# Kernel tuning notes

Measured on AMD Instinct MI355X. Metric: run time of the kernel, lower is better.

## Reference

```python
import jax, jax.numpy as jnp
import numpy as np

THETA = 10000.0


def apply_rope(x, theta):
    # x: [batch, heads, seq, head_dim], head_dim even
    d = x.shape[-1]
    s = x.shape[-2]
    freqs = 1.0 / (theta ** (jnp.arange(0, d, 2, dtype=jnp.float32) / d))  # [d/2]
    pos = jnp.arange(s, dtype=jnp.float32)
    ang = pos[:, None] * freqs[None, :]          # [seq, d/2]
    cos, sin = jnp.cos(ang), jnp.sin(ang)
    x_even = x[..., 0::2]
    x_odd = x[..., 1::2]
    r_even = x_even * cos - x_odd * sin
    r_odd = x_even * sin + x_odd * cos
    # interleave back: [..., seq, d/2, 2] -> [..., seq, d]
    out = jnp.stack([r_even, r_odd], axis=-1).reshape(x.shape)
    return out


def setup_inputs() -> dict:
    key = jax.random.key(0)
    ks = jax.random.split(key, 5)
    B, S, D = 2, 2048, 1024
    scale = 1.0 / np.sqrt(D)
    return {
        "x": jax.random.normal(ks[0], (B, S, D), dtype=jnp.float32),
        "q_proj_weight": jax.random.normal(ks[1], (D, D), dtype=jnp.float32) * scale,
        "k_proj_weight": jax.random.normal(ks[2], (D, D), dtype=jnp.float32) * scale,
        "v_proj_weight": jax.random.normal(ks[3], (D, D), dtype=jnp.float32) * scale,
        "o_proj_weight": jax.random.normal(ks[4], (D, D), dtype=jnp.float32) * scale,
    }


def reference(x, q_proj_weight, k_proj_weight, v_proj_weight, o_proj_weight):
    B, S, D = x.shape
    H = 16
    hd = D // H
    # projections: weight is (d_out, d_in)
    q = jnp.einsum('bsd,ed->bse', x, q_proj_weight)
    k = jnp.einsum('bsd,ed->bse', x, k_proj_weight)
    v = jnp.einsum('bsd,ed->bse', x, v_proj_weight)
    # split heads -> [B, H, S, hd]
    q = q.reshape(B, S, H, hd).transpose(0, 2, 1, 3)
    k = k.reshape(B, S, H, hd).transpose(0, 2, 1, 3)
    v = v.reshape(B, S, H, hd).transpose(0, 2, 1, 3)
    q = apply_rope(q, THETA)
    k = apply_rope(k, THETA)
    scores = jnp.einsum('bhqd,bhkd->bhqk', q, k) / jnp.sqrt(jnp.float32(hd))
    causal = jnp.tril(jnp.ones((S, S), dtype=bool))
    scores = jnp.where(causal, scores, -jnp.inf)
    attn = jax.nn.softmax(scores, axis=-1)
    out = jnp.einsum('bhqk,bhkd->bhqd', attn, v)
    out = out.transpose(0, 2, 1, 3).reshape(B, S, D)
    return jnp.einsum('bsv,dv->bsd', out, o_proj_weight)
```

## Files before the change

### kernel.cpp

```cpp
#include <hip/hip_runtime.h>
#include <hip/hip_bf16.h>
#include <stdint.h>

typedef __attribute__((ext_vector_type(4))) float f32x4;
typedef __attribute__((ext_vector_type(8))) __bf16 bf16x8;
typedef __attribute__((ext_vector_type(4))) __bf16 bf16x4;

#define DEVI __device__ __forceinline__

static constexpr int S_  = 2048;
static constexpr int D_  = 1024;
static constexpr int H_  = 16;
static constexpr int HD_ = 64;
static constexpr int M_  = 2 * S_;
static constexpr float SCL2 = 0.18033688f;

DEVI void gload_lds16(const void* gsrc, void* ldst) {
  __builtin_amdgcn_global_load_lds(
      (__attribute__((address_space(1))) void*)(void*)gsrc,
      (__attribute__((address_space(3))) void*)ldst, 16, 0, 0);
}

DEVI float fexp2(float x) {
  float r;
  asm("v_exp_f32 %0, %1" : "=v"(r) : "v"(x));
  return r;
}

__global__ __launch_bounds__(256) void cvt_all_kernel(
    const float* __restrict__ x, const float* __restrict__ wq,
    const float* __restrict__ wk, const float* __restrict__ wv,
    const float* __restrict__ wo,
    __bf16* __restrict__ xb, __bf16* __restrict__ wqb,
    __bf16* __restrict__ wkb, __bf16* __restrict__ wvb,
    __bf16* __restrict__ wob, float* __restrict__ tab) {
  int blk = blockIdx.x;
  if (blk < 8192) {
    int i = blk * 256 + threadIdx.x;
    const float* src; __bf16* dst; int off;
    if (i < (1 << 20))                      { src = x;  dst = xb;  off = 0; }
    else if (i < (1 << 20) + (1 << 18))     { src = wq; dst = wqb; off = (1 << 20); }
    else if (i < (1 << 20) + 2 * (1 << 18)) { src = wk; dst = wkb; off = (1 << 20) + (1 << 18); }
    else if (i < (1 << 20) + 3 * (1 << 18)) { src = wv; dst = wvb; off = (1 << 20) + 2 * (1 << 18); }
    else                                    { src = wo; dst = wob; off = (1 << 20) + 3 * (1 << 18); }
    int j = i - off;
    float4 v = reinterpret_cast<const float4*>(src)[j];
    bf16x4 o;
    o[0] = (__bf16)v.x; o[1] = (__bf16)v.y; o[2] = (__bf16)v.z; o[3] = (__bf16)v.w;
    reinterpret_cast<bf16x4*>(dst)[j] = o;
  } else {
    int i = (blk - 8192) * 256 + threadIdx.x;
    int s = i >> 5, f = i & 31;
    float freq = powf(10000.0f, -(float)(2 * f) / (float)HD_);
    float ang = (float)s * freq;
    tab[2 * i]     = cosf(ang);
    tab[2 * i + 1] = sinf(ang);
  }
}

__global__ __launch_bounds__(256) void gemm_qkv(
    const __bf16* __restrict__ A, const __bf16* __restrict__ W0,
    const __bf16* __restrict__ W1, const __bf16* __restrict__ W2,
    __bf16* __restrict__ Cq, __bf16* __restrict__ Ck, __bf16* __restrict__ Cvt,
    const float* __restrict__ tab) {
  __shared__ __attribute__((aligned(16))) __bf16 As[128 * 32];
  __shared__ __attribute__((aligned(16))) __bf16 Bs[128 * 32];
  const int tid  = threadIdx.x;
  const int lane = tid & 63;
  const int wv   = tid >> 6;
  const int m0 = blockIdx.x * 128;
  const int n0 = blockIdx.y * 128;
  const int z  = blockIdx.z;
  const __bf16* W = (z == 0) ? W0 : (z == 1 ? W1 : W2);
  const int wm = (wv >> 1) * 64, wn = (wv & 1) * 64;
  const int arow = lane & 15;
  const int kgrp = (lane >> 4) * 8;

  f32x4 acc[4][4];
#pragma unroll
  for (int i = 0; i < 4; i++)
#pragma unroll
    for (int j = 0; j < 4; j++) acc[i][j] = f32x4{0.f, 0.f, 0.f, 0.f};

  for (int k0 = 0; k0 < 1024; k0 += 32) {
    __syncthreads();
#pragma unroll
    for (int j = 0; j < 2; ++j) {
      int c   = (wv * 2 + j) * 64 + lane;
      int row = c >> 2;
      int kc  = (c & 3) * 8;
      gload_lds16(A + (size_t)(m0 + row) * 1024 + k0 + kc,
                  As + (size_t)(wv * 2 + j) * 512);
      gload_lds16(W + (size_t)(n0 + row) * 1024 + k0 + kc,
                  Bs + (size_t)(wv * 2 + j) * 512);
    }
    asm volatile("s_waitcnt vmcnt(0)" ::: "memory");
    __syncthreads();
    bf16x8 af[4], bw[4];
#pragma unroll
    for (int i = 0; i < 4; i++)
      af[i] = *reinterpret_cast<const bf16x8*>(As + (wm + i * 16 + arow) * 32 + kgrp);
#pragma unroll
    for (int i = 0; i < 4; i++)
      bw[i] = *reinterpret_cast<const bf16x8*>(Bs + (wn + i * 16 + arow) * 32 + kgrp);
#pragma unroll
    for (int i = 0; i < 4; i++)
#pragma unroll
      for (int j = 0; j < 4; j++)
        acc[i][j] = __builtin_amdgcn_mfma_f32_16x16x32_bf16(af[i], bw[j], acc[i][j], 0, 0, 0);
  }

  if (z == 2) {
#pragma unroll
    for (int i = 0; i < 4; i++) {
      int m = m0 + wm + i * 16 + (lane >> 4) * 4;
      int bb = m >> 11, srow = m & (S_ - 1);
#pragma unroll
      for (int j = 0; j < 4; j++) {
        int n = n0 + wn + j * 16 + arow;
        int h = n >> 6, d = n & 63;
        bf16x4 o4;
#pragma unroll
        for (int r = 0; r < 4; r++) o4[r] = (__bf16)acc[i][j][r];
        *reinterpret_cast<bf16x4*>(
            Cvt + ((size_t)(bb * H_ + h) * HD_ + d) * S_ + srow) = o4;
      }
    }
  } else {
#pragma unroll
    for (int i = 0; i < 4; i++) {
#pragma unroll
      for (int j = 0; j < 4; j++) {
#pragma unroll
        for (int r = 0; r < 4; r++) {
          int m = m0 + wm + i * 16 + (lane >> 4) * 4 + r;
          int n = n0 + wn + j * 16 + arow;
          float v = acc[i][j][r];
          int bb = m >> 11, srow = m & (S_ - 1);
          int h = n >> 6, d = n & 63;
          size_t oidx = ((size_t)(bb * H_ + h) * S_ + srow) * HD_ + d;
          float other = __shfl_xor(v, 1, 64);
          int fq = d >> 1;
          float2 cssn = *reinterpret_cast<const float2*>(tab + (srow * 32 + fq) * 2);
          float rv = (d & 1) ? (other * cssn.y + v * cssn.x)
                             : (v * cssn.x - other * cssn.y);
          if (z == 0) rv *= SCL2;
          ((z == 0) ? Cq : Ck)[oidx] = (__bf16)rv;
        }
      }
    }
  }
}

__global__ __launch_bounds__(256) void gemm_bt0(
    const __bf16* __restrict__ A, const __bf16* __restrict__ W0,
    float* __restrict__ Cf) {
  constexpr int BK = 32;
  __shared__ __attribute__((aligned(16))) __bf16 As[128 * BK];
  __shared__ __attribute__((aligned(16))) __bf16 Bs[128 * BK];
  const int tid  = threadIdx.x;
  const int lane = tid & 63;
  const int wv   = tid >> 6;
  const int m0 = blockIdx.x * 128;
  const int n0 = blockIdx.y * 128;
  const int wm = (wv >> 1) * 64, wn = (wv & 1) * 64;
  const int arow = lane & 15;
  const int kgrp = (lane >> 4) * 8;

  f32x4 acc[4][4];
#pragma unroll
  for (int i = 0; i < 4; i++)
#pragma unroll
    for (int j = 0; j < 4; j++) acc[i][j] = f32x4{0.f, 0.f, 0.f, 0.f};

  for (int k0 = 0; k0 < 1024; k0 += BK) {
    __syncthreads();
#pragma unroll
    for (int j = 0; j < 2; ++j) {
      int c   = (wv * 2 + j) * 64 + lane;
      int row = c >> 2;
      int kc  = (c & 3) * 8;
      gload_lds16(A + (size_t)(m0 + row) * 1024 + k0 + kc,
                  As + (size_t)(wv * 2 + j) * 512);
      gload_lds16(W0 + (size_t)(n0 + row) * 1024 + k0 + kc,
                  Bs + (size_t)(wv * 2 + j) * 512);
    }
    asm volatile("s_waitcnt vmcnt(0)" ::: "memory");
    __syncthreads();
    bf16x8 af[4], bw[4];
#pragma unroll
    for (int i = 0; i < 4; i++)
      af[i] = *reinterpret_cast<const bf16x8*>(As + (wm + i * 16 + arow) * BK + kgrp);
#pragma unroll
    for (int i = 0; i < 4; i++)
      bw[i] = *reinterpret_cast<const bf16x8*>(Bs + (wn + i * 16 + arow) * BK + kgrp);
#pragma unroll
    for (int i = 0; i < 4; i++)
#pragma unroll
      for (int j = 0; j < 4; j++)
        acc[i][j] = __builtin_amdgcn_mfma_f32_16x16x32_bf16(af[i], bw[j], acc[i][j], 0, 0, 0);
  }

#pragma unroll
  for (int i = 0; i < 4; i++)
#pragma unroll
    for (int j = 0; j < 4; j++)
#pragma unroll
      for (int r = 0; r < 4; r++) {
        int m = m0 + wm + i * 16 + (lane >> 4) * 4 + r;
        int n = n0 + wn + j * 16 + arow;
        Cf[(size_t)m * D_ + n] = acc[i][j][r];
      }
}

__global__ __launch_bounds__(256, 2) void attn_kernel(
    const __bf16* __restrict__ Q, const __bf16* __restrict__ K,
    const __bf16* __restrict__ Vt, __bf16* __restrict__ O) {
  __shared__ __attribute__((aligned(16))) __bf16 Ks[2][128 * 64];
  __shared__ __attribute__((aligned(16))) __bf16 Vs[2][64 * 128];
  const int tid = threadIdx.x, lane = tid & 63, wv = tid >> 6;
  const int bh = blockIdx.x;
  const int pr = blockIdx.y;
  const int b = bh >> 4, h = bh & 15;
  const __bf16* Qb  = Q  + (size_t)bh * S_ * HD_;
  const __bf16* Kb  = K  + (size_t)bh * S_ * HD_;
  const __bf16* Vtb = Vt + (size_t)bh * HD_ * S_;
  const int arow = lane & 15, g = lane >> 4;

#define STAGE(K0, BK_, BV_)                                                   \
  do {                                                                        \
    _Pragma("unroll") for (int j = 0; j < 4; ++j) {                           \
      int c = (wv * 4 + j) * 64 + lane;                    \
      int rowk = c >> 3, qqk = c & 7;                                         \
      int qsk = qqk ^ (rowk & 7);                                             \
      int ctp = rowk >> 4, rw = rowk & 15;                                    \
      int kph = ((ctp & 4) << 4) + ((ctp & 2) << 4) + ((ctp & 1) << 2)        \
                + ((rw >> 2) << 3) + (rw & 3);                                \
      gload_lds16(Kb + (size_t)((K0) + kph) * HD_ + qsk * 8,                  \
                  (BK_) + (size_t)(wv * 4 + j) * 512);                        \
      int rowv = c >> 4, qqv = c & 15;                                        \
      int qsv = qqv ^ (rowv & 7);                                             \
      gload_lds16(Vtb + (size_t)rowv * S_ + (K0) + qsv * 8,                   \
                  (BV_) + (size_t)(wv * 4 + j) * 512);                        \
    }                                                                         \
  } while (0)

  for (int seg = 0; seg < 2; ++seg) {
    const int qt = (seg == 0) ? pr : 31 - pr;
    const int q0 = qt * 64;
    const int nkv = (qt >> 1) + 1;
    const int qw = q0 + wv * 16;
    const int qg = qw + arow;

    bf16x8 aq[2];
#pragma unroll
    for (int j = 0; j < 2; j++)
      aq[j] = *reinterpret_cast<const bf16x8*>(
          Qb + (size_t)(qw + arow) * HD_ + j * 32 + g * 8);

    f32x4 po[4];
#pragma unroll
    for (int dt = 0; dt < 4; dt++) po[dt] = f32x4{0.f, 0.f, 0.f, 0.f};
    float mrow = -1e30f, lrow = 0.f;

    STAGE(0, Ks[0], Vs[0]);
    {
      int t1 = (nkv > 1) ? 128 : 0;
      STAGE(t1, Ks[1], Vs[1]);
    }
    asm volatile("s_waitcnt vmcnt(8)" ::: "memory");
    __builtin_amdgcn_s_barrier();

    for (int kt = 0; kt < nkv; ++kt) {
      const int k0 = kt * 128;
      const int cur = kt & 1;
      const __bf16* Kc = Ks[cur];
      const __bf16* Vc = Vs[cur];

      f32x4 sc4[8];
      __builtin_amdgcn_s_setprio(1);
#pragma unroll
      for (int ct = 0; ct < 8; ct++) {
        sc4[ct] = f32x4{0.f, 0.f, 0.f, 0.f};
        int L = ct * 16 + arow;
#pragma unroll
        for (int j2 = 0; j2 < 2; j2++) {
          int byt = (L * 128 + j2 * 64 + g * 16) ^ ((L & 7) << 4);
          bf16x8 kb = *reinterpret_cast<const bf16x8*>((const char*)Kc + byt);
          sc4[ct] = __builtin_amdgcn_mfma_f32_16x16x32_bf16(kb, aq[j2], sc4[ct], 0, 0, 0);
        }
      }
      __builtin_amdgcn_s_setprio(0);

      if (kt == nkv - 1) {
#pragma unroll
        for (int ct = 0; ct < 8; ct++) {
          int kb0 = k0 + ((ct & 4) << 4) + ((ct & 2) << 4) + ((ct & 1) << 2) + g * 8;
#pragma unroll
          for (int r = 0; r < 4; r++)
            if (kb0 + r > qg) sc4[ct][r] = -1e30f;
        }
      }

      float mx = -1e30f;
#pragma unroll
      for (int ct = 0; ct < 8; ct++)
#pragma unroll
        for (int r = 0; r < 4; r++) mx = fmaxf(mx, sc4[ct][r]);
      mx = fmaxf(mx, __shfl_xor(mx, 16, 64));
      mx = fmaxf(mx, __shfl_xor(mx, 32, 64));

      bool noskip = !__all(mx <= mrow + 11.0f);
      if (noskip) {
        float mnew = fmaxf(mrow, mx);
        float corr = fexp2(mrow - mnew);
        mrow = mnew;
        lrow *= corr;
#pragma unroll
        for (int dt = 0; dt < 4; dt++)
#pragma unroll
          for (int r = 0; r < 4; r++) po[dt][r] *= corr;
      }

      float rs = 0.f;
#pragma unroll
      for (int ct = 0; ct < 8; ct++)
#pragma unroll
        for (int r = 0; r < 4; r++) {
          float e = fexp2(sc4[ct][r] - mrow);
          sc4[ct][r] = e;
          rs += e;
        }
      rs += __shfl_xor(rs, 16, 64);
      rs += __shfl_xor(rs, 32, 64);
      lrow += rs;

      bf16x8 pb[4];
#pragma unroll
      for (int h2 = 0; h2 < 2; h2++)
#pragma unroll
        for (int j2 = 0; j2 < 2; j2++) {
#pragma unroll
          for (int r = 0; r < 4; r++) {
            pb[h2 * 2 + j2][r]     = (__bf16)sc4[h2 * 4 + 2 * j2][r];
            pb[h2 * 2 + j2][4 + r] = (__bf16)sc4[h2 * 4 + 2 * j2 + 1][r];
          }
        }

      __builtin_amdgcn_s_setprio(1);
#pragma unroll
      for (int dt = 0; dt < 4; dt++) {
        int d = dt * 16 + arow;
#pragma unroll
        for (int jj = 0; jj < 4; jj++) {
          int byv = (d * 256 + jj * 64 + g * 16) ^ ((d & 7) << 4);
          bf16x8 vb = *reinterpret_cast<const bf16x8*>((const char*)Vc + byv);
          po[dt] = __builtin_amdgcn_mfma_f32_16x16x32_bf16(vb, pb[jj], po[dt], 0, 0, 0);
        }
      }
      __builtin_amdgcn_s_setprio(0);

      __builtin_amdgcn_s_barrier();
      if (kt < nkv - 1) {
        int nx = kt + 2;
        if (nx > nkv - 1) nx = nkv - 1;
        STAGE(nx * 128, Ks[cur], Vs[cur]);
        asm volatile("s_waitcnt vmcnt(8)" ::: "memory");
      } else {
        asm volatile("s_waitcnt vmcnt(0)" ::: "memory");
      }
      __builtin_amdgcn_s_barrier();
    }

    float inv = __builtin_amdgcn_rcpf(lrow);
#pragma unroll
    for (int dt = 0; dt < 4; dt++) {
      bf16x4 o4;
#pragma unroll
      for (int r = 0; r < 4; r++) o4[r] = (__bf16)(po[dt][r] * inv);
      *reinterpret_cast<bf16x4*>(
          O + (size_t)(b * S_ + qg) * D_ + h * HD_ + dt * 16 + g * 4) = o4;
    }
  }
#undef STAGE
}

extern "C" void kernel_launch(void* const* d_in, const int* in_sizes, int n_in,
                              void* d_out, int out_size, void* d_ws, size_t ws_size,
                              hipStream_t stream) {
  const float* x  = (const float*)d_in[0];
  const float* wq = (const float*)d_in[1];
  const float* wk = (const float*)d_in[2];
  const float* wv = (const float*)d_in[3];
  const float* wo = (const float*)d_in[4];
  float* out = (float*)d_out;

  char* w = (char*)d_ws;
  __bf16* xb  = (__bf16*)(w);
  __bf16* wqb = (__bf16*)(w + (8u  << 20));
  __bf16* wkb = (__bf16*)(w + (10u << 20));
  __bf16* wvb = (__bf16*)(w + (12u << 20));
  __bf16* wob = (__bf16*)(w + (14u << 20));
  __bf16* qws = (__bf16*)(w + (16u << 20));
  __bf16* kws = (__bf16*)(w + (24u << 20));
  __bf16* vtw = (__bf16*)(w + (32u << 20));
  __bf16* aws = (__bf16*)(w + (40u << 20));
  float*  tab = (float*)(w + (48u << 20));

  cvt_all_kernel<<<8448, 256, 0, stream>>>(x, wq, wk, wv, wo,
                                           xb, wqb, wkb, wvb, wob, tab);
  gemm_qkv<<<dim3(32, 8, 3), 256, 0, stream>>>(xb, wqb, wkb, wvb,
                                               qws, kws, vtw, tab);
  attn_kernel<<<dim3(2 * H_, S_ / 128), 256, 0, stream>>>(qws, kws, vtw, aws);
  gemm_bt0<<<dim3(M_ / 128, D_ / 128), 256, 0, stream>>>(aws, wob, out);
}
```

Measured before the change: 120.0 us.

## Use 8 waves per block in QKV and output GEMMs, shrink per-wave tiles

Both projection GEMMs now launch 512 threads (8 waves) per block instead of 256. The QKV GEMM keeps its 128x128 tile and splits it into 64x32 per-wave subtiles. The output GEMM shrinks to a 128x64 tile, doubling the grid, and each wave computes a 32x32 subtile. The aim is more waves in flight and lower register pressure to hide load latency, at the cost of less MFMA work per LDS load and more blocks re-reading A in the output GEMM.

Result: faster. 106.7 us (-11.1%).

```diff
diff --git a/kernel.cpp b/kernel.cpp
--- a/kernel.cpp
+++ b/kernel.cpp
@@ -58,7 +58,7 @@
   }
 }
 
-__global__ __launch_bounds__(256) void gemm_qkv(
+__global__ __launch_bounds__(512, 6) void gemm_qkv(
     const __bf16* __restrict__ A, const __bf16* __restrict__ W0,
     const __bf16* __restrict__ W1, const __bf16* __restrict__ W2,
     __bf16* __restrict__ Cq, __bf16* __restrict__ Ck, __bf16* __restrict__ Cvt,
@@ -68,56 +68,54 @@
   const int tid  = threadIdx.x;
   const int lane = tid & 63;
   const int wv   = tid >> 6;
+  const int wr   = wv >> 2;
+  const int wc   = wv & 3;
   const int m0 = blockIdx.x * 128;
   const int n0 = blockIdx.y * 128;
   const int z  = blockIdx.z;
   const __bf16* W = (z == 0) ? W0 : (z == 1 ? W1 : W2);
-  const int wm = (wv >> 1) * 64, wn = (wv & 1) * 64;
   const int arow = lane & 15;
   const int kgrp = (lane >> 4) * 8;
 
-  f32x4 acc[4][4];
+  f32x4 acc[4][2];
 #pragma unroll
   for (int i = 0; i < 4; i++)
 #pragma unroll
-    for (int j = 0; j < 4; j++) acc[i][j] = f32x4{0.f, 0.f, 0.f, 0.f};
+    for (int j = 0; j < 2; j++) acc[i][j] = f32x4{0.f, 0.f, 0.f, 0.f};
 
   for (int k0 = 0; k0 < 1024; k0 += 32) {
     __syncthreads();
-#pragma unroll
-    for (int j = 0; j < 2; ++j) {
-      int c   = (wv * 2 + j) * 64 + lane;
+    {
+      int c   = wv * 64 + lane;
       int row = c >> 2;
       int kc  = (c & 3) * 8;
-      gload_lds16(A + (size_t)(m0 + row) * 1024 + k0 + kc,
-                  As + (size_t)(wv * 2 + j) * 512);
-      gload_lds16(W + (size_t)(n0 + row) * 1024 + k0 + kc,
-                  Bs + (size_t)(wv * 2 + j) * 512);
+      gload_lds16(A + (size_t)(m0 + row) * 1024 + k0 + kc, As + wv * 512);
+      gload_lds16(W + (size_t)(n0 + row) * 1024 + k0 + kc, Bs + wv * 512);
     }
     asm volatile("s_waitcnt vmcnt(0)" ::: "memory");
     __syncthreads();
-    bf16x8 af[4], bw[4];
+    bf16x8 af[4], bw[2];
 #pragma unroll
     for (int i = 0; i < 4; i++)
-      af[i] = *reinterpret_cast<const bf16x8*>(As + (wm + i * 16 + arow) * 32 + kgrp);
+      af[i] = *reinterpret_cast<const bf16x8*>(As + (wr * 64 + i * 16 + arow) * 32 + kgrp);
+#pragma unroll
+    for (int j = 0; j < 2; j++)
+      bw[j] = *reinterpret_cast<const bf16x8*>(Bs + (wc * 32 + j * 16 + arow) * 32 + kgrp);
 #pragma unroll
     for (int i = 0; i < 4; i++)
-      bw[i] = *reinterpret_cast<const bf16x8*>(Bs + (wn + i * 16 + arow) * 32 + kgrp);
-#pragma unroll
-    for (int i = 0; i < 4; i++)
-#pragma unroll
-      for (int j = 0; j < 4; j++)
+#pragma unroll
+      for (int j = 0; j < 2; j++)
         acc[i][j] = __builtin_amdgcn_mfma_f32_16x16x32_bf16(af[i], bw[j], acc[i][j], 0, 0, 0);
   }
 
   if (z == 2) {
 #pragma unroll
     for (int i = 0; i < 4; i++) {
-      int m = m0 + wm + i * 16 + (lane >> 4) * 4;
+      int m = m0 + wr * 64 + i * 16 + (lane >> 4) * 4;
       int bb = m >> 11, srow = m & (S_ - 1);
 #pragma unroll
-      for (int j = 0; j < 4; j++) {
-        int n = n0 + wn + j * 16 + arow;
+      for (int j = 0; j < 2; j++) {
+        int n = n0 + wc * 32 + j * 16 + arow;
         int h = n >> 6, d = n & 63;
         bf16x4 o4;
 #pragma unroll
@@ -130,11 +128,11 @@
 #pragma unroll
     for (int i = 0; i < 4; i++) {
 #pragma unroll
-      for (int j = 0; j < 4; j++) {
+      for (int j = 0; j < 2; j++) {
 #pragma unroll
         for (int r = 0; r < 4; r++) {
-          int m = m0 + wm + i * 16 + (lane >> 4) * 4 + r;
-          int n = n0 + wn + j * 16 + arow;
+          int m = m0 + wr * 64 + i * 16 + (lane >> 4) * 4 + r;
+          int n = n0 + wc * 32 + j * 16 + arow;
           float v = acc[i][j][r];
           int bb = m >> 11, srow = m & (S_ - 1);
           int h = n >> 6, d = n & 63;
@@ -152,63 +150,61 @@
   }
 }
 
-__global__ __launch_bounds__(256) void gemm_bt0(
+__global__ __launch_bounds__(512, 4) void gemm_bt0(
     const __bf16* __restrict__ A, const __bf16* __restrict__ W0,
     float* __restrict__ Cf) {
-  constexpr int BK = 32;
-  __shared__ __attribute__((aligned(16))) __bf16 As[128 * BK];
-  __shared__ __attribute__((aligned(16))) __bf16 Bs[128 * BK];
+  __shared__ __attribute__((aligned(16))) __bf16 As[128 * 32];
+  __shared__ __attribute__((aligned(16))) __bf16 Bs[64 * 32];
   const int tid  = threadIdx.x;
   const int lane = tid & 63;
   const int wv   = tid >> 6;
+  const int wr   = wv >> 1;
+  const int wc   = wv & 1;
   const int m0 = blockIdx.x * 128;
-  const int n0 = blockIdx.y * 128;
-  const int wm = (wv >> 1) * 64, wn = (wv & 1) * 64;
+  const int n0 = blockIdx.y * 64;
   const int arow = lane & 15;
   const int kgrp = (lane >> 4) * 8;
 
-  f32x4 acc[4][4];
-#pragma unroll
-  for (int i = 0; i < 4; i++)
-#pragma unroll
-    for (int j = 0; j < 4; j++) acc[i][j] = f32x4{0.f, 0.f, 0.f, 0.f};
-
-  for (int k0 = 0; k0 < 1024; k0 += BK) {
+  f32x4 acc[2][2];
+#pragma unroll
+  for (int i = 0; i < 2; i++)
+#pragma unroll
+    for (int j = 0; j < 2; j++) acc[i][j] = f32x4{0.f, 0.f, 0.f, 0.f};
+
+  for (int k0 = 0; k0 < 1024; k0 += 32) {
     __syncthreads();
-#pragma unroll
-    for (int j = 0; j < 2; ++j) {
-      int c   = (wv * 2 + j) * 64 + lane;
+    {
+      int c   = wv * 64 + lane;
       int row = c >> 2;
       int kc  = (c & 3) * 8;
-      gload_lds16(A + (size_t)(m0 + row) * 1024 + k0 + kc,
-                  As + (size_t)(wv * 2 + j) * 512);
-      gload_lds16(W0 + (size_t)(n0 + row) * 1024 + k0 + kc,
-                  Bs + (size_t)(wv * 2 + j) * 512);
+      gload_lds16(A + (size_t)(m0 + row) * 1024 + k0 + kc, As + wv * 512);
+      if (wv < 4)
+        gload_lds16(W0 + (size_t)(n0 + row) * 1024 + k0 + kc, Bs + wv * 512);
     }
     asm volatile("s_waitcnt vmcnt(0)" ::: "memory");
     __syncthreads();
-    bf16x8 af[4], bw[4];
-#pragma unroll
-    for (int i = 0; i < 4; i++)
-      af[i] = *reinterpret_cast<const bf16x8*>(As + (wm + i * 16 + arow) * BK + kgrp);
-#pragma unroll
-    for (int i = 0; i < 4; i++)
-      bw[i] = *reinterpret_cast<const bf16x8*>(Bs + (wn + i * 16 + arow) * BK + kgrp);
-#pragma unroll
-    for (int i = 0; i < 4; i++)
-#pragma unroll
-      for (int j = 0; j < 4; j++)
+    bf16x8 af[2], bw[2];
+#pragma unroll
+    for (int i = 0; i < 2; i++)
+      af[i] = *reinterpret_cast<const bf16x8*>(As + (wr * 32 + i * 16 + arow) * 32 + kgrp);
+#pragma unroll
+    for (int j = 0; j < 2; j++)
+      bw[j] = *reinterpret_cast<const bf16x8*>(Bs + (wc * 32 + j * 16 + arow) * 32 + kgrp);
+#pragma unroll
+    for (int i = 0; i < 2; i++)
+#pragma unroll
+      for (int j = 0; j < 2; j++)
         acc[i][j] = __builtin_amdgcn_mfma_f32_16x16x32_bf16(af[i], bw[j], acc[i][j], 0, 0, 0);
   }
 
 #pragma unroll
-  for (int i = 0; i < 4; i++)
-#pragma unroll
-    for (int j = 0; j < 4; j++)
+  for (int i = 0; i < 2; i++)
+#pragma unroll
+    for (int j = 0; j < 2; j++)
 #pragma unroll
       for (int r = 0; r < 4; r++) {
-        int m = m0 + wm + i * 16 + (lane >> 4) * 4 + r;
-        int n = n0 + wn + j * 16 + arow;
+        int m = m0 + wr * 32 + i * 16 + (lane >> 4) * 4 + r;
+        int n = n0 + wc * 32 + j * 16 + arow;
         Cf[(size_t)m * D_ + n] = acc[i][j][r];
       }
 }
@@ -409,8 +405,8 @@
 
   cvt_all_kernel<<<8448, 256, 0, stream>>>(x, wq, wk, wv, wo,
                                            xb, wqb, wkb, wvb, wob, tab);
-  gemm_qkv<<<dim3(32, 8, 3), 256, 0, stream>>>(xb, wqb, wkb, wvb,
+  gemm_qkv<<<dim3(32, 8, 3), 512, 0, stream>>>(xb, wqb, wkb, wvb,
                                                qws, kws, vtw, tab);
   attn_kernel<<<dim3(2 * H_, S_ / 128), 256, 0, stream>>>(qws, kws, vtw, aws);
-  gemm_bt0<<<dim3(M_ / 128, D_ / 128), 256, 0, stream>>>(aws, wob, out);
-}
+  gemm_bt0<<<dim3(M_ / 128, D_ / 64), 512, 0, stream>>>(aws, wob, out);
+}
```
